# Performance work log

Measured on AMD Instinct MI355X. Metric: run time of the kernel, lower is better.

Reference implementation:

```python
import jax, jax.numpy as jnp
import numpy as np

ORDER = 2  # kernel_size


def setup_inputs() -> dict:
    key = jax.random.key(0)
    ks = jax.random.split(key, 8)
    B, F, N, T, H = 8, 1, 1024, 128, 64
    c_in = (ORDER * 2 + 1) * (2 * F + H)  # 330
    x = jax.random.normal(ks[0], (B, F, N, T), jnp.float32)
    mask = jax.random.randint(ks[1], (B, F, N, T), 0, 2).astype(jnp.bool_)
    adj = jax.random.uniform(ks[2], (N, N), jnp.float32)
    Wr = jax.random.normal(ks[3], (H, c_in), jnp.float32) * 0.05
    Wu = jax.random.normal(ks[4], (H, c_in), jnp.float32) * 0.05
    Wc = jax.random.normal(ks[5], (H, c_in), jnp.float32) * 0.05
    Wout = jax.random.normal(ks[6], (F, H), jnp.float32) * 0.05
    return {"x": x, "mask": mask, "adj": adj,
            "Wr": Wr, "br": jnp.zeros((H,), jnp.float32),
            "Wu": Wu, "bu": jnp.zeros((H,), jnp.float32),
            "Wc": Wc, "bc": jnp.zeros((H,), jnp.float32),
            "Wout": Wout, "bout": jnp.zeros((F,), jnp.float32)}


def reference(x, mask, adj, Wr, br, Wu, bu, Wc, bc, Wout, bout):
    # compute_support: forward/backward row-normalized diffusion matrices
    sup_f = adj / (adj.sum(1, keepdims=True) + 1e-8)
    adj_t = adj.T
    sup_b = adj_t / (adj_t.sum(1, keepdims=True) + 1e-8)
    supports = (sup_f, sup_b)

    def sconv(z, W, b):  # SpatialConvOrderK, z: [B,C,N]
        outs = [z]
        for a in supports:
            z1 = z
            for _ in range(ORDER):
                z1 = jnp.einsum('bcv,wv->bcw', z1, a)
                outs.append(z1)
        zc = jnp.concatenate(outs, axis=1)  # [B, 5*C, N]
        return jnp.einsum('bcn,oc->bon', zc, W) + b[None, :, None]

    def cell(inp, h):  # GCGRUCell
        xh = jnp.concatenate([inp, h], axis=1)
        r = jax.nn.sigmoid(sconv(xh, Wr, br))
        u = jax.nn.sigmoid(sconv(xh, Wu, bu))
        c = jnp.tanh(sconv(jnp.concatenate([inp, r * h], axis=1), Wc, bc))
        return u * h + (1.0 - u) * c

    B, F, N, T = x.shape
    H = Wout.shape[1]
    h0 = jnp.zeros((B, H, N), x.dtype)  # n_nodes=None -> zero init
    xs = jnp.moveaxis(x, -1, 0)    # [T,B,F,N]
    ms = jnp.moveaxis(mask, -1, 0)

    def step(h, xm):
        x_s, m_s = xm
        x_hat = jnp.einsum('bhn,oh->bon', h, Wout) + bout[None, :, None]
        state = h[None]  # n_layers=1 -> [L,B,H,N]
        x_in = jnp.where(m_s, x_s, x_hat)
        inp = jnp.concatenate([x_in, m_s.astype(x_s.dtype)], axis=1)
        return cell(inp, h), (x_hat, state)

    _, (preds, states) = jax.lax.scan(step, h0, (xs, ms))
    predictions = jnp.moveaxis(preds, 0, -1)  # [B,F,N,T]
    states = jnp.moveaxis(states, 0, -1)      # [L,B,H,N,T]
    return predictions, states
```

## Files before the change

kernel.cpp:

```cpp
#include <hip/hip_runtime.h>
#include <math.h>


typedef unsigned short u16;
typedef unsigned int u32;
typedef short bf16x8 __attribute__((ext_vector_type(8)));
typedef float f32x4 __attribute__((ext_vector_type(4)));

#define MFMA16(a, b, c) __builtin_amdgcn_mfma_f32_16x16x32_bf16((a), (b), (c), 0, 0, 0)

#define Bz 8
#define Nn 1024
#define Tt 128
#define Hh 64
#define KC 416
#define CP 80

static __device__ __forceinline__ u16 f2b(float f) {
  u32 u = __float_as_uint(f);
  u = (u + 0x7FFFu + ((u >> 16) & 1u)) >> 16;
  return (u16)u;
}
static __device__ __forceinline__ float b2f(u16 s) { return __uint_as_float(((u32)s) << 16); }
static __device__ __forceinline__ bf16x8 ld8(const u16* p) { return *reinterpret_cast<const bf16x8*>(p); }
static __device__ __forceinline__ void st2f(u16* p, float a, float b) {
  *reinterpret_cast<u32*>(p) = (u32)f2b(a) | ((u32)f2b(b) << 16);
}
static __device__ __forceinline__ void st2u(u16* p, u16 a, u16 b) {
  *reinterpret_cast<u32*>(p) = (u32)a | ((u32)b << 16);
}
static __device__ __forceinline__ float sigm(float x) { return 1.f / (1.f + __expf(-x)); }
static __device__ __forceinline__ float tanh_f(float x) {
  x = fminf(fmaxf(x, -15.f), 15.f);
  float e = __expf(2.f * x);
  return (e - 1.f) / (e + 1.f);
}

__global__ __launch_bounds__(256) void ksums(const float* adj, float* rinv, float* cinv) {
  int id = blockIdx.x * 256 + threadIdx.x;
  if (id < 1024) {
    int w = id;
    float s = 0.f;
    for (int v = 0; v < 1024; ++v) s += adj[v * 1024 + w];
    cinv[w] = 1.f / (s + 1e-8f);
  } else {
    int w = id - 1024;
    float s = 0.f;
    for (int v = 0; v < 1024; ++v) s += adj[w * 1024 + v];
    rinv[w] = 1.f / (s + 1e-8f);
  }
}

__global__ __launch_bounds__(256) void kmakeops(const float* adj, const float* rinv, const float* cinv,
                                                u16* Aops, u16* supft, u16* supbt) {
  int idx = blockIdx.x * 256 + threadIdx.x;
  int w = idx >> 10, v = idx & 1023;
  float a = adj[idx];
  u16 f = f2b(a * rinv[w]);
  u16 bb = f2b(a * cinv[v]);
  Aops[idx] = f;
  supft[v * 1024 + w] = f;
  supbt[idx] = bb;
  Aops[2 * 1048576 + v * 1024 + w] = bb;
}

__global__ __launch_bounds__(256) void kA2(u16* Aops, const u16* supft, const u16* supbt) {
  int wg = blockIdx.x;
  int o2 = wg & 1, mt = (wg >> 1) & 7, ntt = (wg >> 4) & 7;
  const u16* Ab = Aops + (o2 ? 2 * 1048576 : 0);
  const u16* Bb = o2 ? supbt : supft;
  u16* Ob = Aops + (o2 ? 3 * 1048576 : 1048576);
  int tid = threadIdx.x, wave = tid >> 6, lane = tid & 63, l15 = lane & 15, quad = lane >> 4;
  int mbase = mt * 128 + wave * 32;
  f32x4 acc[2][8];
#pragma unroll
  for (int m = 0; m < 2; ++m)
#pragma unroll
    for (int j = 0; j < 8; ++j) acc[m][j] = (f32x4){0.f, 0.f, 0.f, 0.f};
  for (int k = 0; k < 1024; k += 32) {
    int kq = k + quad * 8;
    bf16x8 av[2], bv[8];
#pragma unroll
    for (int m = 0; m < 2; ++m) av[m] = ld8(Ab + (mbase + m * 16 + l15) * 1024 + kq);
#pragma unroll
    for (int j = 0; j < 8; ++j) bv[j] = ld8(Bb + (ntt * 128 + j * 16 + l15) * 1024 + kq);
#pragma unroll
    for (int m = 0; m < 2; ++m)
#pragma unroll
      for (int j = 0; j < 8; ++j) acc[m][j] = MFMA16(av[m], bv[j], acc[m][j]);
  }
#pragma unroll
  for (int m = 0; m < 2; ++m)
#pragma unroll
    for (int j = 0; j < 8; ++j) {
      int v = ntt * 128 + j * 16 + l15;
#pragma unroll
      for (int i = 0; i < 4; ++i) {
        int w = mbase + m * 16 + quad * 4 + i;
        Ob[w * 1024 + v] = f2b(acc[m][j][i]);
      }
    }
}

__global__ __launch_bounds__(256) void kpackw(const float* Wr, const float* Wu, const float* Wc,
                                              u16* Wrup, u16* Wcp) {
  int idx = blockIdx.x * 256 + threadIdx.x;
  int r = idx / KC, k = idx % KC;
  float wv = 0.f;
  if (k < 396) {
    int c = (k < 66) ? k : (k - 66);
    if (r < 64) wv = Wr[r * 330 + c];
    else if (r < 128) wv = Wu[(r - 64) * 330 + c];
    else wv = Wc[(r - 128) * 330 + c];
  }
  if (r < 128) Wrup[r * KC + k] = f2b(wv);
  else Wcp[(r - 128) * KC + k] = f2b(wv);
}

__global__ __launch_bounds__(256) void kstep0(const float* x, const int* mask, const float* bout,
                                              float* h, float* states, float* preds,
                                              u16* xh, u16* xc, u16* zct, u16* yct) {
  int idx = blockIdx.x * 256 + threadIdx.x;
  int b = idx >> 16, o = (idx >> 10) & 63, n = idx & 1023;
  int hidx = (b * 64 + o) * 1024 + n;
  h[hidx] = 0.f;
  states[hidx * 128] = 0.f;
  xh[(b * CP + 2 + o) * 1024 + n] = 0;
  zct[(b * 1024 + n) * KC + 2 + o] = 0;
  zct[(b * 1024 + n) * KC + 68 + o] = 0;
  if (o == 0) {
    int xi = (b * 1024 + n) * 128;
    float xhat = bout[0];
    int mv = mask[xi];
    float xin = mv ? x[xi] : xhat;
    preds[xi] = xhat;
    u16 hi = f2b(xin), lo = f2b(xin - b2f(hi));
    xh[(b * CP + 0) * 1024 + n] = hi;
    xh[(b * CP + 1) * 1024 + n] = f2b((float)mv);
    u16* zr = zct + (b * 1024 + n) * KC;
    zr[0] = hi; zr[1] = f2b((float)mv); zr[66] = lo; zr[67] = 0;
  } else if (o == 1) {
    for (int j = 66; j < 80; ++j) {
      xh[(b * CP + j) * 1024 + n] = 0;
      xc[(b * CP + j) * 1024 + n] = 0;
    }
    u16* zr = zct + (b * 1024 + n) * KC;
    u16* yr = yct + (b * 1024 + n) * KC;
    for (int j = 396; j < KC; ++j) { zr[j] = 0; yr[j] = 0; }
  }
}

__global__ __launch_bounds__(256) void kdiff(const u16* __restrict__ Zin, const u16* __restrict__ Aops,
                                             u16* __restrict__ outT) {
  int wg = blockIdx.x;
  int nth = wg & 1, op = (wg >> 1) & 3, ntl = (wg >> 3) & 3, b = (wg >> 5) & 7;
  int nt = nth * 4 + ntl;
  int tid = threadIdx.x, wave = tid >> 6, lane = tid & 63, l15 = lane & 15, quad = lane >> 4;
  const u16* Zb = Zin + b * CP * 1024;
  const u16* Ab = Aops + op * 1048576;
  int colbase = nt * 128 + wave * 32;
  f32x4 acc[5][2];
#pragma unroll
  for (int m = 0; m < 5; ++m)
#pragma unroll
    for (int j = 0; j < 2; ++j) acc[m][j] = (f32x4){0.f, 0.f, 0.f, 0.f};
  for (int k = 0; k < 1024; k += 32) {
    int kq = k + quad * 8;
    bf16x8 av[5], bv[2];
#pragma unroll
    for (int m = 0; m < 5; ++m) av[m] = ld8(Zb + (m * 16 + l15) * 1024 + kq);
#pragma unroll
    for (int j = 0; j < 2; ++j) bv[j] = ld8(Ab + (colbase + j * 16 + l15) * 1024 + kq);
#pragma unroll
    for (int m = 0; m < 5; ++m)
#pragma unroll
      for (int j = 0; j < 2; ++j) acc[m][j] = MFMA16(av[m], bv[j], acc[m][j]);
  }
  int cbase = 132 + op * 66;
#pragma unroll
  for (int j = 0; j < 2; ++j) {
    int w = colbase + j * 16 + l15;
    u16* orow = outT + (b * 1024 + w) * KC + cbase;
#pragma unroll
    for (int m = 0; m < 5; ++m) {
      int c0 = m * 16 + quad * 4;
      if (c0 < 64) {
        st2f(orow + c0, acc[m][j][0], acc[m][j][1]);
        st2f(orow + c0 + 2, acc[m][j][2], acc[m][j][3]);
      } else if (c0 == 64) {
        st2f(orow + 64, acc[m][j][0], acc[m][j][1]);
      }
    }
  }
}

__global__ __launch_bounds__(256) void kconv_ru(const u16* __restrict__ zct, const u16* __restrict__ Wrup,
                                                const float* br, const float* bu,
                                                const float* __restrict__ h, float* __restrict__ ubuf,
                                                u16* __restrict__ xc, u16* __restrict__ yct) {
  int wg = blockIdx.x;
  int b = wg >> 5, nt = wg & 31;
  int tid = threadIdx.x, wave = tid >> 6, lane = tid & 63, l15 = lane & 15, quad = lane >> 4;
  int obase = wave * 32;
  f32x4 acc[2][2];
#pragma unroll
  for (int m = 0; m < 2; ++m)
#pragma unroll
    for (int j = 0; j < 2; ++j) acc[m][j] = (f32x4){0.f, 0.f, 0.f, 0.f};
  for (int k = 0; k < KC; k += 32) {
    int kq = k + quad * 8;
    bf16x8 av[2], bv[2];
#pragma unroll
    for (int m = 0; m < 2; ++m) av[m] = ld8(Wrup + (obase + m * 16 + l15) * KC + kq);
#pragma unroll
    for (int j = 0; j < 2; ++j) bv[j] = ld8(zct + ((b * 1024 + nt * 32 + j * 16 + l15) * KC + kq));
#pragma unroll
    for (int m = 0; m < 2; ++m)
#pragma unroll
      for (int j = 0; j < 2; ++j) acc[m][j] = MFMA16(av[m], bv[j], acc[m][j]);
  }
#pragma unroll
  for (int m = 0; m < 2; ++m)
#pragma unroll
    for (int j = 0; j < 2; ++j) {
      int o0 = obase + m * 16 + quad * 4;
      int n = nt * 32 + j * 16 + l15;
      if (o0 < 64) {
        u16 hi[4], lo[4];
#pragma unroll
        for (int i = 0; i < 4; ++i) {
          float s = sigm(acc[m][j][i] + br[o0 + i]);
          float rh = s * h[(b * 64 + o0 + i) * 1024 + n];
          hi[i] = f2b(rh);
          lo[i] = f2b(rh - b2f(hi[i]));
          xc[(b * CP + 2 + o0 + i) * 1024 + n] = hi[i];
        }
        u16* yr = yct + (b * 1024 + n) * KC;
        st2u(yr + 2 + o0, hi[0], hi[1]);
        st2u(yr + 4 + o0, hi[2], hi[3]);
        st2u(yr + 68 + o0, lo[0], lo[1]);
        st2u(yr + 70 + o0, lo[2], lo[3]);
      } else {
#pragma unroll
        for (int i = 0; i < 4; ++i)
          ubuf[(b * 64 + o0 - 64 + i) * 1024 + n] = sigm(acc[m][j][i] + bu[o0 - 64 + i]);
      }
    }
  if (tid < 32) {
    int n = nt * 32 + tid;
    const u16* zr = zct + (b * 1024 + n) * KC;
    u16* yr = yct + (b * 1024 + n) * KC;
    yr[0] = zr[0]; yr[1] = zr[1]; yr[66] = zr[66]; yr[67] = zr[67];
    xc[(b * CP + 0) * 1024 + n] = zr[0];
    xc[(b * CP + 1) * 1024 + n] = zr[1];
  }
}

__global__ __launch_bounds__(256) void kconv_c(const u16* __restrict__ yct, const u16* __restrict__ Wcp,
                                               const float* bc, const float* __restrict__ ubuf,
                                               float* __restrict__ h, const float* __restrict__ x,
                                               const int* __restrict__ mask, const float* Wout,
                                               const float* bout, float* __restrict__ preds,
                                               float* __restrict__ states, u16* __restrict__ xh,
                                               u16* __restrict__ zct, int t) {
  __shared__ float lds[64 * 65];
  int wg = blockIdx.x;
  int b = wg >> 4, nt = wg & 15;
  int tid = threadIdx.x, wave = tid >> 6, lane = tid & 63, l15 = lane & 15, quad = lane >> 4;
  int nl = wave * 16 + l15;
  int n = nt * 64 + nl;
  f32x4 acc[4];
#pragma unroll
  for (int m = 0; m < 4; ++m) acc[m] = (f32x4){0.f, 0.f, 0.f, 0.f};
  for (int k = 0; k < KC; k += 32) {
    int kq = k + quad * 8;
    bf16x8 bv = ld8(yct + (b * 1024 + n) * KC + kq);
#pragma unroll
    for (int m = 0; m < 4; ++m) {
      bf16x8 av = ld8(Wcp + (m * 16 + l15) * KC + kq);
      acc[m] = MFMA16(av, bv, acc[m]);
    }
  }
  int t1 = t + 1;
#pragma unroll
  for (int m = 0; m < 4; ++m) {
    int o0 = m * 16 + quad * 4;
    u16 hi[4], lo[4];
#pragma unroll
    for (int i = 0; i < 4; ++i) {
      int o = o0 + i;
      float c = tanh_f(acc[m][i] + bc[o]);
      int idx = (b * 64 + o) * 1024 + n;
      float u = ubuf[idx], hp = h[idx];
      float hn = u * hp + (1.f - u) * c;
      h[idx] = hn;
      lds[o * 65 + nl] = hn;
      hi[i] = f2b(hn);
      lo[i] = f2b(hn - b2f(hi[i]));
      if (t1 < Tt) {
        states[idx * 128 + t1] = hn;
        xh[(b * CP + 2 + o) * 1024 + n] = hi[i];
      }
    }
    if (t1 < Tt) {
      u16* zr = zct + (b * 1024 + n) * KC;
      st2u(zr + 2 + o0, hi[0], hi[1]);
      st2u(zr + 4 + o0, hi[2], hi[3]);
      st2u(zr + 68 + o0, lo[0], lo[1]);
      st2u(zr + 70 + o0, lo[2], lo[3]);
    }
  }
  __syncthreads();
  if (tid < 64 && t1 < Tt) {
    int nn = nt * 64 + tid;
    float xhat = bout[0];
    for (int o = 0; o < 64; ++o) xhat += Wout[o] * lds[o * 65 + tid];
    int xi = (b * 1024 + nn) * 128 + t1;
    int mv = mask[xi];
    float xin = mv ? x[xi] : xhat;
    preds[xi] = xhat;
    u16 hi = f2b(xin), lo = f2b(xin - b2f(hi));
    xh[(b * CP + 0) * 1024 + nn] = hi;
    xh[(b * CP + 1) * 1024 + nn] = f2b((float)mv);
    u16* zr = zct + (b * 1024 + nn) * KC;
    zr[0] = hi; zr[1] = f2b((float)mv); zr[66] = lo; zr[67] = 0;
  }
}

extern "C" void kernel_launch(void* const* d_in, const int* in_sizes, int n_in,
                              void* d_out, int out_size, void* d_ws, size_t ws_size,
                              hipStream_t stream) {
  const float* x = (const float*)d_in[0];
  const int* mask = (const int*)d_in[1];
  const float* adj = (const float*)d_in[2];
  const float* Wr = (const float*)d_in[3];
  const float* br = (const float*)d_in[4];
  const float* Wu = (const float*)d_in[5];
  const float* bu = (const float*)d_in[6];
  const float* Wc = (const float*)d_in[7];
  const float* bc = (const float*)d_in[8];
  const float* Wout = (const float*)d_in[9];
  const float* bout = (const float*)d_in[10];

  float* preds = (float*)d_out;
  float* states = preds + 8 * 1024 * 128;

  u16* Aops = (u16*)d_ws;
  u16* supft = Aops + 4 * 1048576;
  u16* supbt = supft + 1048576;
  float* rinv = (float*)(supbt + 1048576);
  float* cinv = rinv + 1024;
  u16* xh = (u16*)(cinv + 1024);
  u16* xc = xh + Bz * CP * 1024;
  u16* zct = xc + Bz * CP * 1024;
  u16* yct = zct + Bz * 1024 * KC;
  u16* Wrup = yct + Bz * 1024 * KC;
  u16* Wcp = Wrup + 128 * KC;
  float* ubuf = (float*)(Wcp + 64 * KC);
  float* h = ubuf + Bz * 64 * 1024;

  ksums<<<8, 256, 0, stream>>>(adj, rinv, cinv);
  kmakeops<<<4096, 256, 0, stream>>>(adj, rinv, cinv, Aops, supft, supbt);
  kA2<<<128, 256, 0, stream>>>(Aops, supft, supbt);
  kpackw<<<312, 256, 0, stream>>>(Wr, Wu, Wc, Wrup, Wcp);
  kstep0<<<2048, 256, 0, stream>>>(x, mask, bout, h, states, preds, xh, xc, zct, yct);

  for (int t = 0; t < Tt; ++t) {
    kdiff<<<256, 256, 0, stream>>>(xh, Aops, zct);
    kconv_ru<<<256, 256, 0, stream>>>(zct, Wrup, br, bu, h, ubuf, xc, yct);
    kdiff<<<256, 256, 0, stream>>>(xc, Aops, yct);
    kconv_c<<<128, 256, 0, stream>>>(yct, Wcp, bc, ubuf, h, x, mask, Wout, bout,
                                     preds, states, xh, zct, t);
  }
}
```

Before: 12.42 ms.

## Stage time-major states/preds buffers and double grid sizes for per-step kernels

Adds a staged path that transposes x and mask to time-major layout up front. In this path states and preds are written contiguously per step into workspace and transposed back at the end, which replaces the stride-128 scattered stores inside the recurrent loop. Separately, the diffusion and conv kernels are retiled with smaller per-block tiles so each launch uses twice as many workgroups, raising occupancy at the cost of less operand reuse per block. The staged path needs a large extra workspace and falls back to the old layout when the workspace is too small.

```diff
diff --git a/kernel.cpp b/kernel.cpp
--- a/kernel.cpp
+++ b/kernel.cpp
@@ -117,14 +117,32 @@
   else Wcp[(r - 128) * KC + k] = f2b(wv);
 }
 
+__global__ __launch_bounds__(256) void ktr_fwd(const u32* __restrict__ in, u32* __restrict__ out) {
+  __shared__ u32 lds[32 * 129];
+  int wg = blockIdx.x;
+  int nt = wg & 31, b = wg >> 5;
+  int tid = threadIdx.x;
+#pragma unroll
+  for (int p = 0; p < 16; ++p) {
+    int row = p * 2 + (tid >> 7), t = tid & 127;
+    lds[row * 129 + t] = in[(b * 1024 + nt * 32 + row) * 128 + t];
+  }
+  __syncthreads();
+#pragma unroll
+  for (int p = 0; p < 16; ++p) {
+    int t = p * 8 + (tid >> 5), nf = tid & 31;
+    out[(t * 8 + b) * 1024 + nt * 32 + nf] = lds[nf * 129 + t];
+  }
+}
+
 __global__ __launch_bounds__(256) void kstep0(const float* x, const int* mask, const float* bout,
-                                              float* h, float* states, float* preds,
-                                              u16* xh, u16* xc, u16* zct, u16* yct) {
+                                              float* h, float* states_p, float* preds_p,
+                                              u16* xh, u16* xc, u16* zct, u16* yct, int stage) {
   int idx = blockIdx.x * 256 + threadIdx.x;
   int b = idx >> 16, o = (idx >> 10) & 63, n = idx & 1023;
   int hidx = (b * 64 + o) * 1024 + n;
   h[hidx] = 0.f;
-  states[hidx * 128] = 0.f;
+  states_p[stage ? hidx : hidx * 128] = 0.f;
   xh[(b * CP + 2 + o) * 1024 + n] = 0;
   zct[(b * 1024 + n) * KC + 2 + o] = 0;
   zct[(b * 1024 + n) * KC + 68 + o] = 0;
@@ -133,7 +151,7 @@
     float xhat = bout[0];
     int mv = mask[xi];
     float xin = mv ? x[xi] : xhat;
-    preds[xi] = xhat;
+    preds_p[stage ? (b * 1024 + n) : xi] = xhat;
     u16 hi = f2b(xin), lo = f2b(xin - b2f(hi));
     xh[(b * CP + 0) * 1024 + n] = hi;
     xh[(b * CP + 1) * 1024 + n] = f2b((float)mv);
@@ -153,43 +171,34 @@
 __global__ __launch_bounds__(256) void kdiff(const u16* __restrict__ Zin, const u16* __restrict__ Aops,
                                              u16* __restrict__ outT) {
   int wg = blockIdx.x;
-  int nth = wg & 1, op = (wg >> 1) & 3, ntl = (wg >> 3) & 3, b = (wg >> 5) & 7;
-  int nt = nth * 4 + ntl;
+  int op = wg & 3, ct = (wg >> 2) & 15, b = wg >> 6;
   int tid = threadIdx.x, wave = tid >> 6, lane = tid & 63, l15 = lane & 15, quad = lane >> 4;
   const u16* Zb = Zin + b * CP * 1024;
   const u16* Ab = Aops + op * 1048576;
-  int colbase = nt * 128 + wave * 32;
-  f32x4 acc[5][2];
-#pragma unroll
-  for (int m = 0; m < 5; ++m)
-#pragma unroll
-    for (int j = 0; j < 2; ++j) acc[m][j] = (f32x4){0.f, 0.f, 0.f, 0.f};
+  int col = ct * 64 + wave * 16;
+  f32x4 acc[5];
+#pragma unroll
+  for (int m = 0; m < 5; ++m) acc[m] = (f32x4){0.f, 0.f, 0.f, 0.f};
   for (int k = 0; k < 1024; k += 32) {
     int kq = k + quad * 8;
-    bf16x8 av[5], bv[2];
-#pragma unroll
-    for (int m = 0; m < 5; ++m) av[m] = ld8(Zb + (m * 16 + l15) * 1024 + kq);
-#pragma unroll
-    for (int j = 0; j < 2; ++j) bv[j] = ld8(Ab + (colbase + j * 16 + l15) * 1024 + kq);
-#pragma unroll
-    for (int m = 0; m < 5; ++m)
-#pragma unroll
-      for (int j = 0; j < 2; ++j) acc[m][j] = MFMA16(av[m], bv[j], acc[m][j]);
+    bf16x8 bv = ld8(Ab + (col + l15) * 1024 + kq);
+#pragma unroll
+    for (int m = 0; m < 5; ++m) {
+      bf16x8 av = ld8(Zb + (m * 16 + l15) * 1024 + kq);
+      acc[m] = MFMA16(av, bv, acc[m]);
+    }
   }
   int cbase = 132 + op * 66;
-#pragma unroll
-  for (int j = 0; j < 2; ++j) {
-    int w = colbase + j * 16 + l15;
-    u16* orow = outT + (b * 1024 + w) * KC + cbase;
-#pragma unroll
-    for (int m = 0; m < 5; ++m) {
-      int c0 = m * 16 + quad * 4;
-      if (c0 < 64) {
-        st2f(orow + c0, acc[m][j][0], acc[m][j][1]);
-        st2f(orow + c0 + 2, acc[m][j][2], acc[m][j][3]);
-      } else if (c0 == 64) {
-        st2f(orow + 64, acc[m][j][0], acc[m][j][1]);
-      }
+  int n = col + l15;
+  u16* orow = outT + (b * 1024 + n) * KC + cbase;
+#pragma unroll
+  for (int m = 0; m < 5; ++m) {
+    int c0 = m * 16 + quad * 4;
+    if (c0 < 64) {
+      st2f(orow + c0, acc[m][0], acc[m][1]);
+      st2f(orow + c0 + 2, acc[m][2], acc[m][3]);
+    } else if (c0 == 64) {
+      st2f(orow + 64, acc[m][0], acc[m][1]);
     }
   }
 }
@@ -199,92 +208,86 @@
                                                 const float* __restrict__ h, float* __restrict__ ubuf,
                                                 u16* __restrict__ xc, u16* __restrict__ yct) {
   int wg = blockIdx.x;
+  int b = wg >> 6, nt = wg & 63;
+  int tid = threadIdx.x, wave = tid >> 6, lane = tid & 63, l15 = lane & 15, quad = lane >> 4;
+  int obase = wave * 32;
+  int n = nt * 16 + l15;
+  f32x4 acc[2];
+#pragma unroll
+  for (int m = 0; m < 2; ++m) acc[m] = (f32x4){0.f, 0.f, 0.f, 0.f};
+  for (int k = 0; k < KC; k += 32) {
+    int kq = k + quad * 8;
+    bf16x8 bv = ld8(zct + (b * 1024 + n) * KC + kq);
+#pragma unroll
+    for (int m = 0; m < 2; ++m) {
+      bf16x8 av = ld8(Wrup + (obase + m * 16 + l15) * KC + kq);
+      acc[m] = MFMA16(av, bv, acc[m]);
+    }
+  }
+#pragma unroll
+  for (int m = 0; m < 2; ++m) {
+    int o0 = obase + m * 16 + quad * 4;
+    if (o0 < 64) {
+      u16 hi[4], lo[4];
+#pragma unroll
+      for (int i = 0; i < 4; ++i) {
+        float s = sigm(acc[m][i] + br[o0 + i]);
+        float rh = s * h[(b * 64 + o0 + i) * 1024 + n];
+        hi[i] = f2b(rh);
+        lo[i] = f2b(rh - b2f(hi[i]));
+        xc[(b * CP + 2 + o0 + i) * 1024 + n] = hi[i];
+      }
+      u16* yr = yct + (b * 1024 + n) * KC;
+      st2u(yr + 2 + o0, hi[0], hi[1]);
+      st2u(yr + 4 + o0, hi[2], hi[3]);
+      st2u(yr + 68 + o0, lo[0], lo[1]);
+      st2u(yr + 70 + o0, lo[2], lo[3]);
+    } else {
+#pragma unroll
+      for (int i = 0; i < 4; ++i)
+        ubuf[(b * 64 + o0 - 64 + i) * 1024 + n] = sigm(acc[m][i] + bu[o0 - 64 + i]);
+    }
+  }
+  if (tid < 16) {
+    int nn = nt * 16 + tid;
+    const u16* zr = zct + (b * 1024 + nn) * KC;
+    u16* yr = yct + (b * 1024 + nn) * KC;
+    yr[0] = zr[0]; yr[1] = zr[1]; yr[66] = zr[66]; yr[67] = zr[67];
+    xc[(b * CP + 0) * 1024 + nn] = zr[0];
+    xc[(b * CP + 1) * 1024 + nn] = zr[1];
+  }
+}
+
+__global__ __launch_bounds__(256) void kconv_c(const u16* __restrict__ yct, const u16* __restrict__ Wcp,
+                                               const float* bc, const float* __restrict__ ubuf,
+                                               float* __restrict__ h, const float* __restrict__ xsrc,
+                                               const int* __restrict__ msrc, const float* Wout,
+                                               const float* bout, float* __restrict__ preds_p,
+                                               float* __restrict__ states_p, u16* __restrict__ xh,
+                                               u16* __restrict__ zct, int t, int stage) {
+  __shared__ float lds[64 * 33];
+  int wg = blockIdx.x;
   int b = wg >> 5, nt = wg & 31;
   int tid = threadIdx.x, wave = tid >> 6, lane = tid & 63, l15 = lane & 15, quad = lane >> 4;
-  int obase = wave * 32;
-  f32x4 acc[2][2];
-#pragma unroll
-  for (int m = 0; m < 2; ++m)
-#pragma unroll
-    for (int j = 0; j < 2; ++j) acc[m][j] = (f32x4){0.f, 0.f, 0.f, 0.f};
-  for (int k = 0; k < KC; k += 32) {
-    int kq = k + quad * 8;
-    bf16x8 av[2], bv[2];
-#pragma unroll
-    for (int m = 0; m < 2; ++m) av[m] = ld8(Wrup + (obase + m * 16 + l15) * KC + kq);
-#pragma unroll
-    for (int j = 0; j < 2; ++j) bv[j] = ld8(zct + ((b * 1024 + nt * 32 + j * 16 + l15) * KC + kq));
-#pragma unroll
-    for (int m = 0; m < 2; ++m)
-#pragma unroll
-      for (int j = 0; j < 2; ++j) acc[m][j] = MFMA16(av[m], bv[j], acc[m][j]);
-  }
-#pragma unroll
-  for (int m = 0; m < 2; ++m)
-#pragma unroll
-    for (int j = 0; j < 2; ++j) {
-      int o0 = obase + m * 16 + quad * 4;
-      int n = nt * 32 + j * 16 + l15;
-      if (o0 < 64) {
-        u16 hi[4], lo[4];
-#pragma unroll
-        for (int i = 0; i < 4; ++i) {
-          float s = sigm(acc[m][j][i] + br[o0 + i]);
-          float rh = s * h[(b * 64 + o0 + i) * 1024 + n];
-          hi[i] = f2b(rh);
-          lo[i] = f2b(rh - b2f(hi[i]));
-          xc[(b * CP + 2 + o0 + i) * 1024 + n] = hi[i];
-        }
-        u16* yr = yct + (b * 1024 + n) * KC;
-        st2u(yr + 2 + o0, hi[0], hi[1]);
-        st2u(yr + 4 + o0, hi[2], hi[3]);
-        st2u(yr + 68 + o0, lo[0], lo[1]);
-        st2u(yr + 70 + o0, lo[2], lo[3]);
-      } else {
-#pragma unroll
-        for (int i = 0; i < 4; ++i)
-          ubuf[(b * 64 + o0 - 64 + i) * 1024 + n] = sigm(acc[m][j][i] + bu[o0 - 64 + i]);
-      }
-    }
-  if (tid < 32) {
-    int n = nt * 32 + tid;
-    const u16* zr = zct + (b * 1024 + n) * KC;
-    u16* yr = yct + (b * 1024 + n) * KC;
-    yr[0] = zr[0]; yr[1] = zr[1]; yr[66] = zr[66]; yr[67] = zr[67];
-    xc[(b * CP + 0) * 1024 + n] = zr[0];
-    xc[(b * CP + 1) * 1024 + n] = zr[1];
-  }
-}
-
-__global__ __launch_bounds__(256) void kconv_c(const u16* __restrict__ yct, const u16* __restrict__ Wcp,
-                                               const float* bc, const float* __restrict__ ubuf,
-                                               float* __restrict__ h, const float* __restrict__ x,
-                                               const int* __restrict__ mask, const float* Wout,
-                                               const float* bout, float* __restrict__ preds,
-                                               float* __restrict__ states, u16* __restrict__ xh,
-                                               u16* __restrict__ zct, int t) {
-  __shared__ float lds[64 * 65];
-  int wg = blockIdx.x;
-  int b = wg >> 4, nt = wg & 15;
-  int tid = threadIdx.x, wave = tid >> 6, lane = tid & 63, l15 = lane & 15, quad = lane >> 4;
-  int nl = wave * 16 + l15;
-  int n = nt * 64 + nl;
-  f32x4 acc[4];
-#pragma unroll
-  for (int m = 0; m < 4; ++m) acc[m] = (f32x4){0.f, 0.f, 0.f, 0.f};
+  int mp = wave >> 1, nsub = (wave & 1) * 16;
+  int nl = nsub + l15;
+  int n = nt * 32 + nl;
+  f32x4 acc[2];
+#pragma unroll
+  for (int m = 0; m < 2; ++m) acc[m] = (f32x4){0.f, 0.f, 0.f, 0.f};
   for (int k = 0; k < KC; k += 32) {
     int kq = k + quad * 8;
     bf16x8 bv = ld8(yct + (b * 1024 + n) * KC + kq);
 #pragma unroll
-    for (int m = 0; m < 4; ++m) {
-      bf16x8 av = ld8(Wcp + (m * 16 + l15) * KC + kq);
+    for (int m = 0; m < 2; ++m) {
+      bf16x8 av = ld8(Wcp + ((mp * 2 + m) * 16 + l15) * KC + kq);
       acc[m] = MFMA16(av, bv, acc[m]);
     }
   }
   int t1 = t + 1;
 #pragma unroll
-  for (int m = 0; m < 4; ++m) {
-    int o0 = m * 16 + quad * 4;
+  for (int m = 0; m < 2; ++m) {
+    int o0 = (mp * 2 + m) * 16 + quad * 4;
     u16 hi[4], lo[4];
 #pragma unroll
     for (int i = 0; i < 4; ++i) {
@@ -294,11 +297,11 @@
       float u = ubuf[idx], hp = h[idx];
       float hn = u * hp + (1.f - u) * c;
       h[idx] = hn;
-      lds[o * 65 + nl] = hn;
+      lds[o * 33 + nl] = hn;
       hi[i] = f2b(hn);
       lo[i] = f2b(hn - b2f(hi[i]));
       if (t1 < Tt) {
-        states[idx * 128 + t1] = hn;
+        states_p[stage ? (((t1 * 8 + b) * 64 + o) * 1024 + n) : (idx * 128 + t1)] = hn;
         xh[(b * CP + 2 + o) * 1024 + n] = hi[i];
       }
     }
@@ -311,19 +314,55 @@
     }
   }
   __syncthreads();
-  if (tid < 64 && t1 < Tt) {
-    int nn = nt * 64 + tid;
+  if (tid < 32 && t1 < Tt) {
+    int nn = nt * 32 + tid;
     float xhat = bout[0];
-    for (int o = 0; o < 64; ++o) xhat += Wout[o] * lds[o * 65 + tid];
-    int xi = (b * 1024 + nn) * 128 + t1;
-    int mv = mask[xi];
-    float xin = mv ? x[xi] : xhat;
-    preds[xi] = xhat;
+    for (int o = 0; o < 64; ++o) xhat += Wout[o] * lds[o * 33 + tid];
+    int xi = stage ? ((t1 * 8 + b) * 1024 + nn) : ((b * 1024 + nn) * 128 + t1);
+    int mv = msrc[xi];
+    float xin = mv ? xsrc[xi] : xhat;
+    preds_p[xi] = xhat;
     u16 hi = f2b(xin), lo = f2b(xin - b2f(hi));
     xh[(b * CP + 0) * 1024 + nn] = hi;
     xh[(b * CP + 1) * 1024 + nn] = f2b((float)mv);
     u16* zr = zct + (b * 1024 + nn) * KC;
     zr[0] = hi; zr[1] = f2b((float)mv); zr[66] = lo; zr[67] = 0;
+  }
+}
+
+__global__ __launch_bounds__(256) void ktr_states(const float* __restrict__ tmp, float* __restrict__ out) {
+  __shared__ float lds[32 * 129];
+  int wg = blockIdx.x;
+  int nt = wg & 31, o = (wg >> 5) & 63, b = wg >> 11;
+  int tid = threadIdx.x;
+#pragma unroll
+  for (int p = 0; p < 16; ++p) {
+    int t = p * 8 + (tid >> 5), nf = tid & 31;
+    lds[nf * 129 + t] = tmp[((t * 8 + b) * 64 + o) * 1024 + nt * 32 + nf];
+  }
+  __syncthreads();
+#pragma unroll
+  for (int p = 0; p < 16; ++p) {
+    int row = p * 2 + (tid >> 7), t = tid & 127;
+    out[((b * 64 + o) * 1024 + nt * 32 + row) * 128 + t] = lds[row * 129 + t];
+  }
+}
+
+__global__ __launch_bounds__(256) void ktr_preds(const float* __restrict__ tmp, float* __restrict__ out) {
+  __shared__ float lds[32 * 129];
+  int wg = blockIdx.x;
+  int nt = wg & 31, b = wg >> 5;
+  int tid = threadIdx.x;
+#pragma unroll
+  for (int p = 0; p < 16; ++p) {
+    int t = p * 8 + (tid >> 5), nf = tid & 31;
+    lds[nf * 129 + t] = tmp[(t * 8 + b) * 1024 + nt * 32 + nf];
+  }
+  __syncthreads();
+#pragma unroll
+  for (int p = 0; p < 16; ++p) {
+    int row = p * 2 + (tid >> 7), t = tid & 127;
+    out[(b * 1024 + nt * 32 + row) * 128 + t] = lds[row * 129 + t];
   }
 }
 
@@ -345,7 +384,21 @@
   float* preds = (float*)d_out;
   float* states = preds + 8 * 1024 * 128;
 
-  u16* Aops = (u16*)d_ws;
+  const size_t SZ_ST = (size_t)Tt * Bz * Hh * Nn * 4;
+  const size_t SZ_PT = (size_t)Tt * Bz * Nn * 4;
+  const size_t SZ_XT = SZ_PT, SZ_MT = SZ_PT;
+  const size_t SZ_REST = 33198080;
+  const size_t need_staged = SZ_ST + SZ_PT + SZ_XT + SZ_MT + SZ_REST;
+  int stage = (ws_size >= need_staged) ? 1 : 0;
+
+  char* base = (char*)d_ws;
+  float* states_tmp = (float*)base;
+  float* preds_tmp = states_tmp + (size_t)Tt * Bz * Hh * Nn;
+  float* xt = preds_tmp + (size_t)Tt * Bz * Nn;
+  int* mt = (int*)(xt + (size_t)Tt * Bz * Nn);
+  char* rest = stage ? (char*)(mt + (size_t)Tt * Bz * Nn) : base;
+
+  u16* Aops = (u16*)rest;
   u16* supft = Aops + 4 * 1048576;
   u16* supbt = supft + 1048576;
   float* rinv = (float*)(supbt + 1048576);
@@ -359,17 +412,30 @@
   float* ubuf = (float*)(Wcp + 64 * KC);
   float* h = ubuf + Bz * 64 * 1024;
 
+  float* states_p = stage ? states_tmp : states;
+  float* preds_p = stage ? preds_tmp : preds;
+  const float* xsrc = stage ? (const float*)xt : x;
+  const int* msrc = stage ? (const int*)mt : mask;
+
   ksums<<<8, 256, 0, stream>>>(adj, rinv, cinv);
   kmakeops<<<4096, 256, 0, stream>>>(adj, rinv, cinv, Aops, supft, supbt);
   kA2<<<128, 256, 0, stream>>>(Aops, supft, supbt);
   kpackw<<<312, 256, 0, stream>>>(Wr, Wu, Wc, Wrup, Wcp);
-  kstep0<<<2048, 256, 0, stream>>>(x, mask, bout, h, states, preds, xh, xc, zct, yct);
+  if (stage) {
+    ktr_fwd<<<256, 256, 0, stream>>>((const u32*)x, (u32*)xt);
+    ktr_fwd<<<256, 256, 0, stream>>>((const u32*)mask, (u32*)mt);
+  }
+  kstep0<<<2048, 256, 0, stream>>>(x, mask, bout, h, states_p, preds_p, xh, xc, zct, yct, stage);
 
   for (int t = 0; t < Tt; ++t) {
-    kdiff<<<256, 256, 0, stream>>>(xh, Aops, zct);
-    kconv_ru<<<256, 256, 0, stream>>>(zct, Wrup, br, bu, h, ubuf, xc, yct);
-    kdiff<<<256, 256, 0, stream>>>(xc, Aops, yct);
-    kconv_c<<<128, 256, 0, stream>>>(yct, Wcp, bc, ubuf, h, x, mask, Wout, bout,
-                                     preds, states, xh, zct, t);
-  }
-}
+    kdiff<<<512, 256, 0, stream>>>(xh, Aops, zct);
+    kconv_ru<<<512, 256, 0, stream>>>(zct, Wrup, br, bu, h, ubuf, xc, yct);
+    kdiff<<<512, 256, 0, stream>>>(xc, Aops, yct);
+    kconv_c<<<256, 256, 0, stream>>>(yct, Wcp, bc, ubuf, h, xsrc, msrc, Wout, bout,
+                                     preds_p, states_p, xh, zct, t, stage);
+  }
+  if (stage) {
+    ktr_states<<<16384, 256, 0, stream>>>(states_tmp, states);
+    ktr_preds<<<256, 256, 0, stream>>>(preds_tmp, preds);
+  }
+}
```

After: 14.43 ms. 1.16x slower.
